# Kernel tuning notes

Measured on AMD Instinct MI355X. Metric: run time of the kernel, lower is better.

## Reference

```python
import jax, jax.numpy as jnp
import numpy as np

B, S, D, H, DH = 2, 2048, 1024, 16, 64
LN_EPS = 1e-5

def _layernorm(x, g, b):
    mu = jnp.mean(x, axis=-1, keepdims=True)
    var = jnp.mean(jnp.square(x - mu), axis=-1, keepdims=True)
    return (x - mu) * jax.lax.rsqrt(var + LN_EPS) * g + b

def setup_inputs() -> dict:
    key = jax.random.key(0)
    ks = jax.random.split(key, 12)
    s = 0.02
    return {
        'x': jax.random.normal(ks[0], (B, S, D), jnp.float32),
        'attention_mask': jnp.zeros((B, S), jnp.bool_),
        'Wq': jax.random.normal(ks[1], (H, D, DH), jnp.float32) * s,
        'bq': jnp.zeros((H, DH), jnp.float32),
        'Wk': jax.random.normal(ks[2], (H, D, DH), jnp.float32) * s,
        'bk': jnp.zeros((H, DH), jnp.float32),
        'Wv': jax.random.normal(ks[3], (H, D, DH), jnp.float32) * s,
        'bv': jnp.zeros((H, DH), jnp.float32),
        'ln_g': jnp.ones((D,), jnp.float32),
        'ln_b': jnp.zeros((D,), jnp.float32),
        'W1': jax.random.normal(ks[4], (D, 4 * D), jnp.float32) * s,
        'b1': jnp.zeros((4 * D,), jnp.float32),
        'W2': jax.random.normal(ks[5], (4 * D, D), jnp.float32) * s,
        'b2': jnp.zeros((D,), jnp.float32),
    }

def reference(x, attention_mask, Wq, bq, Wk, bk, Wv, bv, ln_g, ln_b, W1, b1, W2, b2):
    # NOTE: source has a typo bug ('attentoin_score'), so the attention_mask is
    # computed-then-discarded; softmax is applied to the UNMASKED scaled scores.
    dh = Wq.shape[-1]
    q = jnp.einsum('bsd,hde->bhse', x, Wq) + bq[:, None, :]  # [B,H,S,dh]
    k = jnp.einsum('bsd,hde->bhse', x, Wk) + bk[:, None, :]
    v = jnp.einsum('bsd,hde->bhse', x, Wv) + bv[:, None, :]
    scores = jnp.einsum('bhse,bhte->bhst', q, k) / jnp.sqrt(jnp.float32(dh))
    attn = jax.nn.softmax(scores, axis=-1)
    o = jnp.einsum('bhst,bhte->bhse', attn, v)  # [B,H,S,dh]
    b_, h_, s_, e_ = o.shape
    # concat heads along last dim == transpose then reshape
    mha = jnp.transpose(o, (0, 2, 1, 3)).reshape(b_, s_, h_ * e_)
    h1 = _layernorm(x + mha, ln_g, ln_b)
    ffn = jax.nn.relu(h1 @ W1 + b1) @ W2 + b2
    return _layernorm(h1 + ffn, ln_g, ln_b)
```

## Files before the change

### kernel.cpp

```cpp
#include <hip/hip_runtime.h>

#define DEVI __device__ __forceinline__

typedef __attribute__((ext_vector_type(8))) __bf16 bf16x8;
typedef __attribute__((ext_vector_type(4))) float f32x4;
typedef __attribute__((ext_vector_type(4))) unsigned short u16x4;
typedef __attribute__((ext_vector_type(8))) unsigned short u16x8;

static DEVI unsigned short f2bf(float f) {
  unsigned int i = __float_as_uint(f);
  i += 0x7fffu + ((i >> 16) & 1u);
  return (unsigned short)(i >> 16);
}

static DEVI unsigned short f2bfh(float f) {
  union { __bf16 h; unsigned short u; } c;
  c.h = (__bf16)f;
  return c.u;
}

static DEVI float bf2f(unsigned short u) {
  return __uint_as_float((unsigned int)u << 16);
}

static DEVI f32x4 mfma16x16x32(bf16x8 a, bf16x8 b, f32x4 c) {
  return __builtin_amdgcn_mfma_f32_16x16x32_bf16(a, b, c, 0, 0, 0);
}

static DEVI void async_ld16(const void* g, void* lds) {
  __builtin_amdgcn_global_load_lds(
      (const __attribute__((address_space(1))) void*)g,
      (__attribute__((address_space(3))) void*)lds, 16, 0, 0);
}

static DEVI void wg_barrier() {
  __asm__ volatile("" ::: "memory");
  __builtin_amdgcn_s_barrier();
  __asm__ volatile("" ::: "memory");
}

template <int OUT_MODE, bool RELU>
static DEVI void gemm256_core(const unsigned short* __restrict__ A, int lda,
                              const unsigned short* __restrict__ Bt, int ldb,
                              int m0, int n0, const float* __restrict__ bias,
                              void* __restrict__ Cp, int ldc,
                              const float* __restrict__ bq,
                              const float* __restrict__ bk,
                              const float* __restrict__ bv,
                              unsigned short* __restrict__ qo,
                              unsigned short* __restrict__ ko,
                              unsigned short* __restrict__ vo) {
  constexpr int NKT = 16;
  __shared__ __align__(16) unsigned short As[2][16384];
  __shared__ __align__(16) unsigned short Bs[2][16384];

  const int tid = threadIdx.x;
  const int w = tid >> 6, l = tid & 63;
  const int lr = l & 15, lq = l >> 4;
  const int wm = w >> 2, wn = w & 3;

  const int srow = tid >> 3;
  const int scol = ((tid & 7) ^ (srow & 7)) << 3;
  const unsigned short* sA = A + (size_t)(m0 + srow) * lda + scol;
  const unsigned short* sB = Bt + (size_t)(n0 + srow) * ldb + scol;
  unsigned short* dA = &As[0][0] + w * 512;
  unsigned short* dB = &Bs[0][0] + w * 512;

  auto stA = [&](int c, int h, int kb) {
    const unsigned short* s = sA + (size_t)h * 128 * lda + kb;
    unsigned short* d = dA + c * 16384 + h * 8192;
    async_ld16(s, d);
    async_ld16(s + (size_t)64 * lda, d + 4096);
  };
  auto stB = [&](int c, int h, int kb) {
    const unsigned short* s = sB + (size_t)h * 128 * ldb + kb;
    unsigned short* d = dB + c * 16384 + h * 8192;
    async_ld16(s, d);
    async_ld16(s + (size_t)64 * ldb, d + 4096);
  };

  stA(0, 0, 0); stB(0, 0, 0); stB(0, 1, 0); stA(0, 1, 0);
  stA(1, 0, 64); stB(1, 0, 64); stB(1, 1, 64);

  f32x4 acc[8][4];
#pragma unroll
  for (int i = 0; i < 8; ++i)
#pragma unroll
    for (int j = 0; j < 4; ++j) acc[i][j] = (f32x4){0.f, 0.f, 0.f, 0.f};

  const int frow = wm * 16 + lr;
  const int brow = wn * 16 + lr;
  const int g0 = (lq ^ (lr & 7)) << 3;
  const int g1 = ((4 + lq) ^ (lr & 7)) << 3;

  bf16x8 af[4][2], bf[2][2][2];

  auto mfma_quad = [&](int qm, int qn) {
    __builtin_amdgcn_s_setprio(1);
#pragma unroll
    for (int m = 0; m < 4; ++m)
#pragma unroll
      for (int n = 0; n < 2; ++n) {
        f32x4 t = acc[qm * 4 + m][qn * 2 + n];
        t = mfma16x16x32(af[m][0], bf[qn][n][0], t);
        t = mfma16x16x32(af[m][1], bf[qn][n][1], t);
        acc[qm * 4 + m][qn * 2 + n] = t;
      }
    __builtin_amdgcn_s_setprio(0);
  };

  asm volatile("s_waitcnt vmcnt(6)" ::: "memory");
  wg_barrier();

  for (int kt = 0; kt < NKT; ++kt) {
    const int c = kt & 1;
    const unsigned short* Ac = &As[c][0];
    const unsigned short* Bc = &Bs[c][0];
    const int kb1 = (kt + 1) * 64, kb2 = (kt + 2) * 64;

#pragma unroll
    for (int m = 0; m < 4; ++m) {
      const unsigned short* p = Ac + (frow + m * 32) * 64;
      af[m][0] = *(const bf16x8*)(p + g0);
      af[m][1] = *(const bf16x8*)(p + g1);
    }
#pragma unroll
    for (int n = 0; n < 2; ++n) {
      const unsigned short* p = Bc + (brow + n * 64) * 64;
      bf[0][n][0] = *(const bf16x8*)(p + g0);
      bf[0][n][1] = *(const bf16x8*)(p + g1);
    }
    if (kt + 1 < NKT) stA(c ^ 1, 1, kb1);
    wg_barrier();
    mfma_quad(0, 0);
    wg_barrier();

#pragma unroll
    for (int n = 0; n < 2; ++n) {
      const unsigned short* p = Bc + (128 + brow + n * 64) * 64;
      bf[1][n][0] = *(const bf16x8*)(p + g0);
      bf[1][n][1] = *(const bf16x8*)(p + g1);
    }
    if (kt + 2 < NKT) stA(c, 0, kb2);
    wg_barrier();
    mfma_quad(0, 1);
    wg_barrier();

#pragma unroll
    for (int m = 0; m < 4; ++m) {
      const unsigned short* p = Ac + (128 + frow + m * 32) * 64;
      af[m][0] = *(const bf16x8*)(p + g0);
      af[m][1] = *(const bf16x8*)(p + g1);
    }
    if (kt + 2 < NKT) stB(c, 0, kb2);
    wg_barrier();
    mfma_quad(1, 0);
    wg_barrier();

    if (kt + 2 < NKT) stB(c, 1, kb2);
    wg_barrier();
    mfma_quad(1, 1);
    if (kt < NKT - 2)
      asm volatile("s_waitcnt vmcnt(6)" ::: "memory");
    else
      asm volatile("s_waitcnt vmcnt(0)" ::: "memory");
    wg_barrier();
  }

#pragma unroll
  for (int qm = 0; qm < 2; ++qm)
#pragma unroll
    for (int m = 0; m < 4; ++m) {
      const int grow = m0 + qm * 128 + wm * 16 + m * 32 + lq * 4;
#pragma unroll
      for (int qn = 0; qn < 2; ++qn)
#pragma unroll
        for (int n = 0; n < 2; ++n) {
          const int gcol = n0 + qn * 128 + wn * 16 + n * 64 + lr;
          const f32x4 av = acc[qm * 4 + m][qn * 2 + n];
          if (OUT_MODE == 2) {
            const int which = gcol >> 10;
            const int h = (gcol >> 6) & 15;
            const int e = gcol & 63;
            const float* bp = (which == 0) ? bq : (which == 1) ? bk : bv;
            const float bvv = bp[gcol & 1023];
#pragma unroll
            for (int r = 0; r < 4; ++r) {
              const int row = grow + r;
              const int b_ = row >> 11, s_ = row & 2047;
              const size_t base = (size_t)((b_ << 4) + h) * 131072;
              const float val = av[r] + bvv;
              if (which == 0) {
                qo[base + (size_t)s_ * 64 + e] = f2bf(val);
              } else if (which == 1) {
                const int o = e >> 3;
                const int pos = (((o ^ (s_ & 7)) << 3) | (e & 7));
                ko[base + (size_t)s_ * 64 + pos] = f2bf(val * 0.18033688011112f);
              } else {
                const int t = s_ >> 6, k64 = s_ & 63;
                const int kap = (k64 & 15) * 4 + (k64 >> 4);
                const int pos = (((kap >> 3) ^ (e & 7)) << 3) | (kap & 7);
                vo[base + (size_t)e * 2048 + t * 64 + pos] = f2bf(val);
              }
            }
          } else if (OUT_MODE == 3) {
#pragma unroll
            for (int r = 0; r < 4; ++r)
              ((unsigned short*)Cp)[(size_t)(grow + r) * ldc + gcol] =
                  f2bf(av[r]);
          } else {
            const float bvv = bias[gcol];
#pragma unroll
            for (int r = 0; r < 4; ++r) {
              float val = av[r] + bvv;
              if (RELU) val = fmaxf(val, 0.f);
              ((unsigned short*)Cp)[(size_t)(grow + r) * ldc + gcol] = f2bf(val);
            }
          }
        }
    }
}

__global__ __launch_bounds__(512, 2) void k_gemm_qkv(
    const unsigned short* __restrict__ xb, const unsigned short* __restrict__ Wt,
    const float* __restrict__ bq, const float* __restrict__ bk,
    const float* __restrict__ bv, unsigned short* __restrict__ qo,
    unsigned short* __restrict__ ko, unsigned short* __restrict__ vo) {
  const int bid = blockIdx.x;
  const int xcd = bid & 7, idx = bid >> 3;
  const int mt = (xcd >> 1) * 4 + idx / 6;
  const int nt = (xcd & 1) * 6 + idx % 6;
  gemm256_core<2, false>(xb, 1024, Wt, 1024, mt * 256, nt * 256, nullptr,
                         nullptr, 0, bq, bk, bv, qo, ko, vo);
}

__global__ __launch_bounds__(512, 2) void k_ffn1(
    const unsigned short* __restrict__ h1b, const unsigned short* __restrict__ W1t,
    const float* __restrict__ b1, unsigned short* __restrict__ f1) {
  const int bid = blockIdx.x;
  const int xcd = bid & 7, idx = bid >> 3;
  const int mt = (xcd >> 1) * 4 + (idx >> 3);
  const int nt = (xcd & 1) * 8 + (idx & 7);
  gemm256_core<1, true>(h1b, 1024, W1t, 1024, mt * 256, nt * 256, b1, f1, 4096,
                        nullptr, nullptr, nullptr, nullptr, nullptr, nullptr);
}

__global__ __launch_bounds__(512, 2) void k_ffn2(
    const unsigned short* __restrict__ f1, const unsigned short* __restrict__ W2t,
    unsigned short* __restrict__ pbase) {
  const int z = blockIdx.z;
  unsigned short* p = pbase + (size_t)z * 4194304;
  const int bid = blockIdx.x;
  const int xcd = bid & 7, idx = bid >> 3;
  const int mt = xcd * 2 + (idx >> 2);
  const int nt = idx & 3;
  gemm256_core<3, false>(f1 + z * 1024, 4096, W2t + z * 1024, 4096, mt * 256,
                         nt * 256, nullptr, p, 1024, nullptr, nullptr, nullptr,
                         nullptr, nullptr, nullptr);
}

static DEVI void tr64(const float* __restrict__ s, int sld,
                      unsigned short* __restrict__ d, int dld) {
  __shared__ float t[64][65];
  const int tr = threadIdx.x >> 4;
  const int tc4 = (threadIdx.x & 15) * 4;
#pragma unroll
  for (int i = 0; i < 4; ++i) {
    f32x4 v = *(const f32x4*)(s + (size_t)(i * 16 + tr) * sld + tc4);
#pragma unroll
    for (int j = 0; j < 4; ++j) t[i * 16 + tr][tc4 + j] = v[j];
  }
  __syncthreads();
#pragma unroll
  for (int i = 0; i < 4; ++i) {
    const int c = i * 16 + tr;
    u16x4 pk;
#pragma unroll
    for (int j = 0; j < 4; ++j) pk[j] = f2bf(t[tc4 + j][c]);
    *(u16x4*)(d + (size_t)c * dld + tc4) = pk;
  }
}

__global__ __launch_bounds__(256) void k_prep(
    const float* __restrict__ x, const float* __restrict__ Wq,
    const float* __restrict__ Wk, const float* __restrict__ Wv,
    const float* __restrict__ W1, const float* __restrict__ W2,
    unsigned short* __restrict__ xb, unsigned short* __restrict__ wqkvt,
    unsigned short* __restrict__ w1t, unsigned short* __restrict__ w2t) {
  const int bid = blockIdx.x;
  if (bid < 1024) {
    const size_t i0 = ((size_t)bid * 256 + threadIdx.x) * 16;
#pragma unroll
    for (int c = 0; c < 4; ++c) {
      f32x4 v = *(const f32x4*)(x + i0 + c * 4);
      u16x4 pk;
#pragma unroll
      for (int j = 0; j < 4; ++j) pk[j] = f2bf(v[j]);
      *(u16x4*)(xb + i0 + c * 4) = pk;
    }
  } else if (bid < 1792) {
    const int t = bid - 1024;
    const int bx = t & 15, by = t >> 4;
    const int which = by >> 4, h = by & 15;
    const float* W = (which == 0) ? Wq : (which == 1) ? Wk : Wv;
    const float* s = W + (size_t)h * 65536;
    unsigned short* d = wqkvt + (size_t)(which * 1024 + h * 64) * 1024;
    const int r0 = bx * 64;
    tr64(s + (size_t)r0 * 64, 64, d + r0, 1024);
  } else if (bid < 2816) {
    const int t = bid - 1792;
    const int bx = t & 15, by = t >> 4;
    const int r0 = bx * 64, c0 = by * 64;
    tr64(W1 + (size_t)r0 * 4096 + c0, 4096, w1t + (size_t)c0 * 1024 + r0, 1024);
  } else {
    const int t = bid - 2816;
    const int bx = t & 63, by = t >> 6;
    const int r0 = bx * 64, c0 = by * 64;
    tr64(W2 + (size_t)r0 * 1024 + c0, 1024, w2t + (size_t)c0 * 4096 + r0, 4096);
  }
}

__global__ __launch_bounds__(512) void k_attn(
    const unsigned short* __restrict__ q, const unsigned short* __restrict__ ks,
    const unsigned short* __restrict__ vp, unsigned short* __restrict__ mha) {
  const int bid = blockIdx.x;
  const int bh = (bid & 7) * 4 + ((bid >> 3) >> 4);
  const int qt = (bid >> 3) & 15;
  const int b = bh >> 4, h = bh & 15;
  const int tid = threadIdx.x;
  const int w = tid >> 6, l = tid & 63;
  const int lr = l & 15, lq = l >> 4, l7 = lr & 7;

  __shared__ __align__(16) unsigned short Ks[2][64 * 64];
  __shared__ __align__(16) unsigned short Vt[2][64 * 64];
  __shared__ __align__(16) unsigned short Ps[8][16][72];

  const size_t bho = (size_t)bh * 131072;
  const int q0 = qt * 128 + w * 16;

  bf16x8 qf0, qf1;
  {
    const unsigned short* qp = q + bho + (size_t)(q0 + lr) * 64 + lq * 8;
    qf0 = *(const bf16x8*)qp;
    qf1 = *(const bf16x8*)(qp + 32);
  }

  f32x4 l_acc[4];
  f32x4 o[4];
#pragma unroll
  for (int i = 0; i < 4; ++i) {
    l_acc[i] = (f32x4){0.f, 0.f, 0.f, 0.f};
    o[i] = (f32x4){0.f, 0.f, 0.f, 0.f};
  }

  const unsigned short* kg = ks + bho;
  const unsigned short* vg = vp + bho;
  const int srow = l >> 3, scol = (l & 7) * 8;
  const int r0 = w * 8;

  async_ld16(kg + (size_t)(r0 + srow) * 64 + scol, &Ks[0][r0 * 64]);
  async_ld16(vg + (size_t)(r0 + srow) * 2048 + scol, &Vt[0][r0 * 64]);
  __syncthreads();

  for (int kt = 0; kt < 32; ++kt) {
    const int cur = kt & 1, nxt = cur ^ 1;
    if (kt + 1 < 32) {
      const int k1 = (kt + 1) * 64;
      async_ld16(kg + (size_t)(k1 + r0 + srow) * 64 + scol, &Ks[nxt][r0 * 64]);
      async_ld16(vg + (size_t)(r0 + srow) * 2048 + k1 + scol, &Vt[nxt][r0 * 64]);
    }

    bf16x8 kf[4][2];
#pragma unroll
    for (int ct = 0; ct < 4; ++ct)
#pragma unroll
      for (int hh = 0; hh < 2; ++hh)
        kf[ct][hh] = *(const bf16x8*)&Ks[cur][(ct * 16 + lr) * 64 +
                                             (((hh << 2) | lq) ^ l7) * 8];
    f32x4 s[4];
#pragma unroll
    for (int ct = 0; ct < 4; ++ct) {
      f32x4 t = {0.f, 0.f, 0.f, 0.f};
      t = mfma16x16x32(qf0, kf[ct][0], t);
      t = mfma16x16x32(qf1, kf[ct][1], t);
      s[ct] = t;
    }

#pragma unroll
    for (int r = 0; r < 4; ++r) {
      f32x4 pe;
#pragma unroll
      for (int ct = 0; ct < 4; ++ct)
        pe[ct] = __builtin_amdgcn_exp2f(s[ct][r]);
      l_acc[r] += pe;
      u16x4 pk;
#pragma unroll
      for (int ct = 0; ct < 4; ++ct) pk[ct] = f2bfh(pe[ct]);
      *(u16x4*)&Ps[w][lq * 4 + r][lr * 4] = pk;
    }
    __asm__ volatile("" ::: "memory");

    bf16x8 vf[4][2];
#pragma unroll
    for (int dt = 0; dt < 4; ++dt)
#pragma unroll
      for (int hh = 0; hh < 2; ++hh)
        vf[dt][hh] = *(const bf16x8*)&Vt[cur][(dt * 16 + lr) * 64 +
                                             (((hh << 2) | lq) ^ l7) * 8];
    bf16x8 pf0 = *(const bf16x8*)&Ps[w][lr][lq * 8];
    bf16x8 pf1 = *(const bf16x8*)&Ps[w][lr][32 + lq * 8];
#pragma unroll
    for (int dt = 0; dt < 4; ++dt) {
      o[dt] = mfma16x16x32(pf0, vf[dt][0], o[dt]);
      o[dt] = mfma16x16x32(pf1, vf[dt][1], o[dt]);
    }
    __syncthreads();
  }

#pragma unroll
  for (int r = 0; r < 4; ++r) {
    f32x4 la = l_acc[r];
    float sd = la[0] + la[1] + la[2] + la[3];
    sd += __shfl_xor(sd, 1);
    sd += __shfl_xor(sd, 2);
    sd += __shfl_xor(sd, 4);
    sd += __shfl_xor(sd, 8);
    const float inv = 1.f / sd;
    unsigned short* op =
        mha + ((size_t)b * 2048 + q0 + lq * 4 + r) * 1024 + h * 64 + lr;
    op[0] = f2bfh(o[0][r] * inv);
    op[16] = f2bfh(o[1][r] * inv);
    op[32] = f2bfh(o[2][r] * inv);
    op[48] = f2bfh(o[3][r] * inv);
  }
}

__global__ __launch_bounds__(256) void k_add_ln(const float* __restrict__ a,
                                                const unsigned short* __restrict__ b,
                                                const float* __restrict__ g,
                                                const float* __restrict__ be,
                                                unsigned short* __restrict__ outb) {
  const int row = blockIdx.x;
  const int tid = threadIdx.x;
  const size_t base = (size_t)row * 1024 + tid * 4;
  f32x4 va = *(const f32x4*)(a + base);
  u16x4 ub = *(const u16x4*)(b + base);
  f32x4 xx;
  float s = 0.f, q = 0.f;
#pragma unroll
  for (int i = 0; i < 4; ++i) {
    xx[i] = va[i] + bf2f(ub[i]);
    s += xx[i];
    q += xx[i] * xx[i];
  }
#pragma unroll
  for (int off = 1; off < 64; off <<= 1) {
    s += __shfl_xor(s, off);
    q += __shfl_xor(q, off);
  }
  __shared__ float ss[4], qs[4];
  const int w = tid >> 6;
  if ((tid & 63) == 0) { ss[w] = s; qs[w] = q; }
  __syncthreads();
  s = ss[0] + ss[1] + ss[2] + ss[3];
  q = qs[0] + qs[1] + qs[2] + qs[3];
  const float mean = s * (1.f / 1024.f);
  const float var = q * (1.f / 1024.f) - mean * mean;
  const float rstd = rsqrtf(var + 1e-5f);
  f32x4 vg = *(const f32x4*)(g + tid * 4);
  f32x4 vbe = *(const f32x4*)(be + tid * 4);
  u16x4 pk;
#pragma unroll
  for (int i = 0; i < 4; ++i)
    pk[i] = f2bf((xx[i] - mean) * rstd * vg[i] + vbe[i]);
  *(u16x4*)(outb + base) = pk;
}

__global__ __launch_bounds__(256) void k_add_ln4(
    const unsigned short* __restrict__ h1b, const unsigned short* __restrict__ pb,
    const float* __restrict__ cb, const float* __restrict__ g,
    const float* __restrict__ be, float* __restrict__ out) {
  const int row = blockIdx.x;
  const int tid = threadIdx.x;
  const size_t base = (size_t)row * 1024 + tid * 4;
  u16x4 uh = *(const u16x4*)(h1b + base);
  u16x4 up[4];
#pragma unroll
  for (int z = 0; z < 4; ++z)
    up[z] = *(const u16x4*)(pb + base + (size_t)z * 4194304);
  f32x4 vcb = *(const f32x4*)(cb + tid * 4);
  f32x4 xx;
  float s = 0.f, q = 0.f;
#pragma unroll
  for (int i = 0; i < 4; ++i) {
    float v = bf2f(uh[i]) + vcb[i];
#pragma unroll
    for (int z = 0; z < 4; ++z) v += bf2f(up[z][i]);
    xx[i] = v;
    s += v;
    q += v * v;
  }
#pragma unroll
  for (int off = 1; off < 64; off <<= 1) {
    s += __shfl_xor(s, off);
    q += __shfl_xor(q, off);
  }
  __shared__ float ss[4], qs[4];
  const int w = tid >> 6;
  if ((tid & 63) == 0) { ss[w] = s; qs[w] = q; }
  __syncthreads();
  s = ss[0] + ss[1] + ss[2] + ss[3];
  q = qs[0] + qs[1] + qs[2] + qs[3];
  const float mean = s * (1.f / 1024.f);
  const float var = q * (1.f / 1024.f) - mean * mean;
  const float rstd = rsqrtf(var + 1e-5f);
  f32x4 vg = *(const f32x4*)(g + tid * 4);
  f32x4 vbe = *(const f32x4*)(be + tid * 4);
  f32x4 ov;
#pragma unroll
  for (int i = 0; i < 4; ++i) ov[i] = (xx[i] - mean) * rstd * vg[i] + vbe[i];
  *(f32x4*)(out + base) = ov;
}

extern "C" void kernel_launch(void* const* d_in, const int* in_sizes, int n_in,
                              void* d_out, int out_size, void* d_ws,
                              size_t ws_size, hipStream_t stream) {
  const float* x = (const float*)d_in[0];
  const float* Wq = (const float*)d_in[2];
  const float* bq = (const float*)d_in[3];
  const float* Wk = (const float*)d_in[4];
  const float* bk = (const float*)d_in[5];
  const float* Wv = (const float*)d_in[6];
  const float* bv = (const float*)d_in[7];
  const float* lg = (const float*)d_in[8];
  const float* lb = (const float*)d_in[9];
  const float* W1 = (const float*)d_in[10];
  const float* b1 = (const float*)d_in[11];
  const float* W2 = (const float*)d_in[12];
  const float* b2 = (const float*)d_in[13];

  char* ws = (char*)d_ws;
  const size_t MB = 1024 * 1024;
  unsigned short* qb = (unsigned short*)(ws + 0);
  unsigned short* kb = (unsigned short*)(ws + 8 * MB);
  unsigned short* vp = (unsigned short*)(ws + 16 * MB);
  unsigned short* f1 = (unsigned short*)(ws + 0);
  unsigned short* xb = (unsigned short*)(ws + 32 * MB);
  unsigned short* pb = (unsigned short*)(ws + 32 * MB);
  unsigned short* mha = (unsigned short*)(ws + 40 * MB);
  unsigned short* h1b = (unsigned short*)(ws + 64 * MB);
  unsigned short* wqkvt = (unsigned short*)(ws + 72 * MB);
  unsigned short* w1t = (unsigned short*)(ws + 78 * MB);
  unsigned short* w2t = (unsigned short*)(ws + 86 * MB);

  k_prep<<<dim3(3840), 256, 0, stream>>>(x, Wq, Wk, Wv, W1, W2, xb, wqkvt, w1t,
                                         w2t);
  k_gemm_qkv<<<dim3(192), 512, 0, stream>>>(xb, wqkvt, bq, bk, bv, qb, kb, vp);
  k_attn<<<dim3(512), 512, 0, stream>>>(qb, kb, vp, mha);
  k_add_ln<<<dim3(4096), 256, 0, stream>>>(x, mha, lg, lb, h1b);
  k_ffn1<<<dim3(256), 512, 0, stream>>>(h1b, w1t, b1, f1);
  k_ffn2<<<dim3(64, 1, 4), 512, 0, stream>>>(f1, w2t, pb);
  k_add_ln4<<<dim3(4096), 256, 0, stream>>>(h1b, pb, b2, lg, lb, (float*)d_out);
}
```

Before: 306.3 us.

## Simplify GEMM main loop to single-stage double buffering without LDS swizzle

Replaces the fine-grained interleaved pipeline (staggered A/B half-tile loads two steps ahead, per-quadrant barriers, s_setprio, explicit vmcnt waits) with a simple loop. Each iteration issues all loads for the next k-tile, computes the current tile, then runs one __syncthreads. It also drops the XOR swizzle on LDS rows, so fragment reads use plain lq*8 offsets. This cuts barrier count and code complexity, but risks LDS bank conflicts and less overlap of global loads with MFMA. Correctness also relies on __syncthreads waiting on the async LDS loads.

```diff
diff --git a/kernel.cpp b/kernel.cpp
--- a/kernel.cpp
+++ b/kernel.cpp
@@ -31,12 +31,6 @@
   __builtin_amdgcn_global_load_lds(
       (const __attribute__((address_space(1))) void*)g,
       (__attribute__((address_space(3))) void*)lds, 16, 0, 0);
-}
-
-static DEVI void wg_barrier() {
-  __asm__ volatile("" ::: "memory");
-  __builtin_amdgcn_s_barrier();
-  __asm__ volatile("" ::: "memory");
 }
 
 template <int OUT_MODE, bool RELU>
@@ -60,27 +54,21 @@
   const int wm = w >> 2, wn = w & 3;
 
   const int srow = tid >> 3;
-  const int scol = ((tid & 7) ^ (srow & 7)) << 3;
+  const int scol = (tid & 7) << 3;
   const unsigned short* sA = A + (size_t)(m0 + srow) * lda + scol;
   const unsigned short* sB = Bt + (size_t)(n0 + srow) * ldb + scol;
   unsigned short* dA = &As[0][0] + w * 512;
   unsigned short* dB = &Bs[0][0] + w * 512;
 
-  auto stA = [&](int c, int h, int kb) {
-    const unsigned short* s = sA + (size_t)h * 128 * lda + kb;
-    unsigned short* d = dA + c * 16384 + h * 8192;
-    async_ld16(s, d);
-    async_ld16(s + (size_t)64 * lda, d + 4096);
+  auto stageAll = [&](int c, int kb) {
+#pragma unroll
+    for (int q = 0; q < 4; ++q) {
+      async_ld16(sA + (size_t)(q * 64) * lda + kb, dA + c * 16384 + q * 4096);
+      async_ld16(sB + (size_t)(q * 64) * ldb + kb, dB + c * 16384 + q * 4096);
+    }
   };
-  auto stB = [&](int c, int h, int kb) {
-    const unsigned short* s = sB + (size_t)h * 128 * ldb + kb;
-    unsigned short* d = dB + c * 16384 + h * 8192;
-    async_ld16(s, d);
-    async_ld16(s + (size_t)64 * ldb, d + 4096);
-  };
-
-  stA(0, 0, 0); stB(0, 0, 0); stB(0, 1, 0); stA(0, 1, 0);
-  stA(1, 0, 64); stB(1, 0, 64); stB(1, 1, 64);
+
+  stageAll(0, 0);
 
   f32x4 acc[8][4];
 #pragma unroll
@@ -90,81 +78,62 @@
 
   const int frow = wm * 16 + lr;
   const int brow = wn * 16 + lr;
-  const int g0 = (lq ^ (lr & 7)) << 3;
-  const int g1 = ((4 + lq) ^ (lr & 7)) << 3;
-
-  bf16x8 af[4][2], bf[2][2][2];
-
-  auto mfma_quad = [&](int qm, int qn) {
-    __builtin_amdgcn_s_setprio(1);
-#pragma unroll
-    for (int m = 0; m < 4; ++m)
-#pragma unroll
-      for (int n = 0; n < 2; ++n) {
-        f32x4 t = acc[qm * 4 + m][qn * 2 + n];
-        t = mfma16x16x32(af[m][0], bf[qn][n][0], t);
-        t = mfma16x16x32(af[m][1], bf[qn][n][1], t);
-        acc[qm * 4 + m][qn * 2 + n] = t;
-      }
-    __builtin_amdgcn_s_setprio(0);
-  };
-
-  asm volatile("s_waitcnt vmcnt(6)" ::: "memory");
-  wg_barrier();
+
+  __syncthreads();
 
   for (int kt = 0; kt < NKT; ++kt) {
     const int c = kt & 1;
+    if (kt + 1 < NKT) stageAll(c ^ 1, (kt + 1) * 64);
+
     const unsigned short* Ac = &As[c][0];
     const unsigned short* Bc = &Bs[c][0];
-    const int kb1 = (kt + 1) * 64, kb2 = (kt + 2) * 64;
+    bf16x8 af[4][2], bf[2][2][2];
 
 #pragma unroll
     for (int m = 0; m < 4; ++m) {
-      const unsigned short* p = Ac + (frow + m * 32) * 64;
-      af[m][0] = *(const bf16x8*)(p + g0);
-      af[m][1] = *(const bf16x8*)(p + g1);
-    }
-#pragma unroll
-    for (int n = 0; n < 2; ++n) {
-      const unsigned short* p = Bc + (brow + n * 64) * 64;
-      bf[0][n][0] = *(const bf16x8*)(p + g0);
-      bf[0][n][1] = *(const bf16x8*)(p + g1);
-    }
-    if (kt + 1 < NKT) stA(c ^ 1, 1, kb1);
-    wg_barrier();
-    mfma_quad(0, 0);
-    wg_barrier();
-
-#pragma unroll
-    for (int n = 0; n < 2; ++n) {
-      const unsigned short* p = Bc + (128 + brow + n * 64) * 64;
-      bf[1][n][0] = *(const bf16x8*)(p + g0);
-      bf[1][n][1] = *(const bf16x8*)(p + g1);
-    }
-    if (kt + 2 < NKT) stA(c, 0, kb2);
-    wg_barrier();
-    mfma_quad(0, 1);
-    wg_barrier();
+      const unsigned short* p = Ac + (frow + m * 32) * 64 + lq * 8;
+      af[m][0] = *(const bf16x8*)p;
+      af[m][1] = *(const bf16x8*)(p + 32);
+    }
+#pragma unroll
+    for (int qn = 0; qn < 2; ++qn)
+#pragma unroll
+      for (int n = 0; n < 2; ++n) {
+        const unsigned short* p = Bc + (qn * 128 + brow + n * 64) * 64 + lq * 8;
+        bf[qn][n][0] = *(const bf16x8*)p;
+        bf[qn][n][1] = *(const bf16x8*)(p + 32);
+      }
+#pragma unroll
+    for (int m = 0; m < 4; ++m)
+#pragma unroll
+      for (int qn = 0; qn < 2; ++qn)
+#pragma unroll
+        for (int n = 0; n < 2; ++n) {
+          f32x4 t = acc[m][qn * 2 + n];
+          t = mfma16x16x32(af[m][0], bf[qn][n][0], t);
+          t = mfma16x16x32(af[m][1], bf[qn][n][1], t);
+          acc[m][qn * 2 + n] = t;
+        }
 
 #pragma unroll
     for (int m = 0; m < 4; ++m) {
-      const unsigned short* p = Ac + (128 + frow + m * 32) * 64;
-      af[m][0] = *(const bf16x8*)(p + g0);
-      af[m][1] = *(const bf16x8*)(p + g1);
-    }
-    if (kt + 2 < NKT) stB(c, 0, kb2);
-    wg_barrier();
-    mfma_quad(1, 0);
-    wg_barrier();
-
-    if (kt + 2 < NKT) stB(c, 1, kb2);
-    wg_barrier();
-    mfma_quad(1, 1);
-    if (kt < NKT - 2)
-      asm volatile("s_waitcnt vmcnt(6)" ::: "memory");
-    else
-      asm volatile("s_waitcnt vmcnt(0)" ::: "memory");
-    wg_barrier();
+      const unsigned short* p = Ac + (128 + frow + m * 32) * 64 + lq * 8;
+      af[m][0] = *(const bf16x8*)p;
+      af[m][1] = *(const bf16x8*)(p + 32);
+    }
+#pragma unroll
+    for (int m = 0; m < 4; ++m)
+#pragma unroll
+      for (int qn = 0; qn < 2; ++qn)
+#pragma unroll
+        for (int n = 0; n < 2; ++n) {
+          f32x4 t = acc[4 + m][qn * 2 + n];
+          t = mfma16x16x32(af[m][0], bf[qn][n][0], t);
+          t = mfma16x16x32(af[m][1], bf[qn][n][1], t);
+          acc[4 + m][qn * 2 + n] = t;
+        }
+
+    __syncthreads();
   }
 
 #pragma unroll
```

Result: slower. 348.7 us (+13.9%).
